# Optimization experiments

Measured on AMD Instinct MI355X. Metric: run time of the kernel, lower is better.

Reference implementation:

```python
import jax, jax.numpy as jnp
import numpy as np

D_MODEL = 128
N_HEADS = 8
D_K = D_MODEL // N_HEADS
N_TGT = 40000
N_SRC = 40000
N_EDGES = 640000


def setup_inputs() -> dict:
    key = jax.random.key(0)
    ks = jax.random.split(key, 12)
    s = 1.0 / np.sqrt(D_MODEL)
    return {
        "X_tgt": jax.random.normal(ks[0], (N_TGT, D_MODEL), jnp.float32),
        "X_src": jax.random.normal(ks[1], (N_SRC, D_MODEL), jnp.float32),
        "inc_tgt": jax.random.randint(ks[2], (N_EDGES,), 0, N_TGT),
        "inc_src": jax.random.randint(ks[3], (N_EDGES,), 0, N_SRC),
        "num_tgt": N_TGT,
        # weights stored (in, out): y = x @ W
        "Wq": jax.random.normal(ks[4], (D_MODEL, D_MODEL), jnp.float32) * s,
        "Wkv": jax.random.normal(ks[5], (D_MODEL, 2 * D_MODEL), jnp.float32) * s,
        "Wbt": jax.random.normal(ks[6], (D_MODEL, N_HEADS), jnp.float32) * s,
        "Wbs": jax.random.normal(ks[7], (D_MODEL, N_HEADS), jnp.float32) * s,
        "Wgt_w": jax.random.normal(ks[8], (D_MODEL, D_MODEL), jnp.float32) * s,
        "Wgt_b": jnp.zeros((D_MODEL,), jnp.float32),
        "Wgs_w": jax.random.normal(ks[9], (D_MODEL, D_MODEL), jnp.float32) * s,
        "Wgs_b": jnp.zeros((D_MODEL,), jnp.float32),
        "Wo": jax.random.normal(ks[10], (D_MODEL, D_MODEL), jnp.float32) * s,
    }


def reference(X_tgt, X_src, inc_tgt, inc_src, num_tgt, Wq, Wkv, Wbt, Wbs,
              Wgt_w, Wgt_b, Wgs_w, Wgs_b, Wo):
    H, dk = N_HEADS, D_K
    scale = 1.0 / np.sqrt(dk)
    n_src = X_src.shape[0]

    Q = (X_tgt @ Wq).reshape(-1, H, dk)                 # [Nt,H,dk]
    kv = (X_src @ Wkv).reshape(n_src, 2, H, dk)
    K, V = kv[:, 0], kv[:, 1]                           # [Ns,H,dk]

    # per-edge attention scores [E,H]
    scores = (jnp.sum(Q[inc_tgt] * K[inc_src], axis=-1) * scale
              + (X_tgt @ Wbt)[inc_tgt]
              + (X_src @ Wbs)[inc_src])

    # segment softmax over edges grouped by target node
    mx = jax.ops.segment_max(scores, inc_tgt, num_segments=num_tgt)  # [Nt,H]
    exp_s = jnp.exp(scores - mx[inc_tgt])
    sm = jax.ops.segment_sum(exp_s, inc_tgt, num_segments=num_tgt)
    attn = exp_s / (sm[inc_tgt] + 1e-12)                # [E,H]

    g_src = jax.nn.sigmoid(X_src @ Wgs_w + Wgs_b).reshape(n_src, H, dk)
    msg = attn[..., None] * (g_src[inc_src] * V[inc_src])          # [E,H,dk]
    out = jax.ops.segment_sum(msg, inc_tgt, num_segments=num_tgt)  # [Nt,H,dk]

    g_tgt = jax.nn.sigmoid(X_tgt @ Wgt_w + Wgt_b).reshape(-1, H, dk)
    return (g_tgt * out).reshape(-1, H * dk) @ Wo
```

## Files before the change

kernel.cpp:

```cpp
#include <hip/hip_runtime.h>
#include <math.h>

#define NTGT 40000
#define NSRC 40000
#define NEDGE 640000
#define LOG2E 1.44269504088896f
#define KGROW 256
#define CAP 64

typedef __attribute__((ext_vector_type(8))) short bfrag;
typedef __attribute__((ext_vector_type(4))) short bhalf4;
typedef __attribute__((ext_vector_type(8))) short bhalf8;
typedef __attribute__((ext_vector_type(4))) float f4acc;

__device__ __forceinline__ ushort f2bf(float f) {
  uint u = __float_as_uint(f);
  u += 0x7fffu + ((u >> 16) & 1u);
  return (ushort)(u >> 16);
}
__device__ __forceinline__ float bflo(uint u) { return __uint_as_float(u << 16); }
__device__ __forceinline__ float bfhi(uint u) { return __uint_as_float(u & 0xffff0000u); }
__device__ __forceinline__ float bf2f(short s) { return __uint_as_float(((uint)(ushort)s) << 16); }
__device__ __forceinline__ float sigmoidf_fast(float x) { return 1.0f / (1.0f + __expf(-x)); }

__global__ __launch_bounds__(256) void k_prep(const float* __restrict__ Wq,
                                              const float* __restrict__ Wkv,
                                              const float* __restrict__ Wgt_w,
                                              const float* __restrict__ Wgs_w,
                                              const float* __restrict__ Wo,
                                              const float* __restrict__ Wbt,
                                              const float* __restrict__ Wbs,
                                              int* __restrict__ cnt,
                                              short* __restrict__ WqT, short* __restrict__ WkT,
                                              short* __restrict__ WvT, short* __restrict__ WgtT,
                                              short* __restrict__ WgsT, short* __restrict__ WoT,
                                              short* __restrict__ WbtT, short* __restrict__ WbsT) {
  const int b = blockIdx.x;
  const int tid = threadIdx.x;
  if (b >= 8) {
    int i = (b - 8) * 256 + tid;
    if (i < NTGT) cnt[i] = 0;
    return;
  }
  if (b >= 6) {
    const float* src = (b == 6) ? Wbt : Wbs;
    short* dst = (b == 6) ? WbtT : WbsT;
    for (int idx = tid; idx < 16 * 128; idx += 256) {
      int n = idx >> 7, k = idx & 127;
      dst[idx] = (n < 8) ? (short)f2bf(src[k * 8 + n]) : (short)0;
    }
    return;
  }
  __shared__ short T[128][136];
  const float* src;
  int ld, off;
  short* dst;
  switch (b) {
    case 0: src = Wq;    ld = 128; off = 0;   dst = WqT;  break;
    case 1: src = Wkv;   ld = 256; off = 0;   dst = WkT;  break;
    case 2: src = Wkv;   ld = 256; off = 128; dst = WvT;  break;
    case 3: src = Wgt_w; ld = 128; off = 0;   dst = WgtT; break;
    case 4: src = Wgs_w; ld = 128; off = 0;   dst = WgsT; break;
    default:src = Wo;    ld = 128; off = 0;   dst = WoT;  break;
  }
  for (int i = tid; i < 128 * 32; i += 256) {
    int k = i >> 5, c4 = (i & 31) * 4;
    float4 v = *reinterpret_cast<const float4*>(src + (size_t)k * ld + off + c4);
    T[c4 + 0][k] = (short)f2bf(v.x);
    T[c4 + 1][k] = (short)f2bf(v.y);
    T[c4 + 2][k] = (short)f2bf(v.z);
    T[c4 + 3][k] = (short)f2bf(v.w);
  }
  __syncthreads();
  for (int u = tid; u < 128 * 16; u += 256) {
    int n = u >> 4, o = (u & 15) * 8;
    *reinterpret_cast<bhalf8*>(dst + (size_t)n * 128 + o) =
        *reinterpret_cast<const bhalf8*>(&T[n][o]);
  }
}

__global__ __launch_bounds__(512) void k_fill(const int* __restrict__ inc_tgt,
                                              const int* __restrict__ inc_src,
                                              int* __restrict__ cnt,
                                              int* __restrict__ elist) {
  int e = blockIdx.x * 512 + threadIdx.x;
  int t = inc_tgt[e];
  int pos = atomicAdd(&cnt[t], 1);
  pos = min(pos, CAP - 1);
  elist[t * CAP + pos] = inc_src[e];
}

#define MFMA16(a, b, c) __builtin_amdgcn_mfma_f32_16x16x32_bf16(a, b, c, 0, 0, 0)

__device__ __forceinline__ void stage_issue(const float* __restrict__ X, size_t row0,
                                            float4 ld[4], int tid) {
#pragma unroll
  for (int it = 0; it < 4; ++it) {
    int i = it * 512 + tid;
    int r = i >> 5, c4 = (i & 31) * 4;
    ld[it] = *reinterpret_cast<const float4*>(X + (row0 + r) * 128 + c4);
  }
}
__device__ __forceinline__ void stage_write(short (*Xs)[136], const float4 ld[4], int tid) {
#pragma unroll
  for (int it = 0; it < 4; ++it) {
    int i = it * 512 + tid;
    int r = i >> 5, c4 = (i & 31) * 4;
    bhalf4 o;
    o[0] = (short)f2bf(ld[it].x); o[1] = (short)f2bf(ld[it].y);
    o[2] = (short)f2bf(ld[it].z); o[3] = (short)f2bf(ld[it].w);
    *reinterpret_cast<bhalf4*>(&Xs[r][c4]) = o;
  }
}

__global__ __launch_bounds__(512) void k_proj(const float* __restrict__ Xt,
                                              const float* __restrict__ Xsrc,
                                              const short* __restrict__ WqT,
                                              const short* __restrict__ WgtT,
                                              const short* __restrict__ WkT,
                                              const short* __restrict__ WvT,
                                              const short* __restrict__ WgsT,
                                              const short* __restrict__ WbtT,
                                              const short* __restrict__ WbsT,
                                              const float* __restrict__ Wgt_b,
                                              const float* __restrict__ Wgs_b,
                                              short* __restrict__ Qb, short* __restrict__ gtb,
                                              float* __restrict__ bt16,
                                              short* __restrict__ KG,
                                              short* __restrict__ bsb) {
  __shared__ short Xs[64][136];
  __shared__ short Stg[64][256];
  const int tid = threadIdx.x;
  const int w = tid >> 6, lane = tid & 63;
  const int nl = lane & 15;
  const int kg = (lane >> 4) * 8;
  const int r4 = (lane >> 4) * 4;
  const int c0 = w * 16;
  const bool is_src = blockIdx.x >= 125;
  const int t0 = (is_src ? blockIdx.x - 125 : blockIdx.x) * 5;
  const float* X = is_src ? Xsrc : Xt;

  if (!is_src) {
    bfrag Bq[4], Bg[4], Bb[4];
#pragma unroll
    for (int ks = 0; ks < 4; ++ks) {
      const size_t wo = (size_t)(c0 + nl) * 128 + ks * 32 + kg;
      Bq[ks] = *reinterpret_cast<const bfrag*>(WqT + wo);
      Bg[ks] = *reinterpret_cast<const bfrag*>(WgtT + wo);
      Bb[ks] = *reinterpret_cast<const bfrag*>(WbtT + (size_t)nl * 128 + ks * 32 + kg);
    }
    const int c = c0 + nl;
    const float gb = Wgt_b[c];
    {
      float4 ld[4];
      stage_issue(X, (size_t)t0 * 64, ld, tid);
      stage_write(Xs, ld, tid);
    }
    __syncthreads();
    for (int ti = 0; ti < 5; ++ti) {
      const size_t row0 = (size_t)(t0 + ti) * 64;
      float4 ld[4];
      if (ti < 4) stage_issue(X, row0 + 64, ld, tid);
      f4acc aQ[4] = {}, aG[4] = {}, aB[4] = {};
#pragma unroll
      for (int ks = 0; ks < 4; ++ks) {
        const int ko = ks * 32 + kg;
        bfrag a0 = *reinterpret_cast<const bfrag*>(&Xs[nl][ko]);
        bfrag a1 = *reinterpret_cast<const bfrag*>(&Xs[16 + nl][ko]);
        bfrag a2 = *reinterpret_cast<const bfrag*>(&Xs[32 + nl][ko]);
        bfrag a3 = *reinterpret_cast<const bfrag*>(&Xs[48 + nl][ko]);
        aQ[0] = MFMA16(a0, Bq[ks], aQ[0]);
        aQ[1] = MFMA16(a1, Bq[ks], aQ[1]);
        aQ[2] = MFMA16(a2, Bq[ks], aQ[2]);
        aQ[3] = MFMA16(a3, Bq[ks], aQ[3]);
        aG[0] = MFMA16(a0, Bg[ks], aG[0]);
        aG[1] = MFMA16(a1, Bg[ks], aG[1]);
        aG[2] = MFMA16(a2, Bg[ks], aG[2]);
        aG[3] = MFMA16(a3, Bg[ks], aG[3]);
        if (w == 0) {
          aB[0] = MFMA16(a0, Bb[ks], aB[0]);
          aB[1] = MFMA16(a1, Bb[ks], aB[1]);
          aB[2] = MFMA16(a2, Bb[ks], aB[2]);
          aB[3] = MFMA16(a3, Bb[ks], aB[3]);
        }
      }
#pragma unroll
      for (int rf = 0; rf < 4; ++rf)
#pragma unroll
        for (int j = 0; j < 4; ++j) {
          int r = rf * 16 + r4 + j;
          Stg[r][c] = (short)f2bf(aQ[rf][j] * (0.25f * LOG2E));
          Stg[r][128 + c] = (short)f2bf(sigmoidf_fast(aG[rf][j] + gb));
        }
      if (w == 0) {
#pragma unroll
        for (int rf = 0; rf < 4; ++rf)
#pragma unroll
          for (int j = 0; j < 4; ++j)
            bt16[(row0 + rf * 16 + r4 + j) * 16 + nl] = aB[rf][j] * LOG2E;
      }
      __syncthreads();
      if (ti < 4) stage_write(Xs, ld, tid);
      for (int u = tid; u < 1024; u += 512) {
        int r = u >> 4, o = (u & 15) * 8;
        *reinterpret_cast<bhalf8*>(Qb + (row0 + r) * 128 + o) =
            *reinterpret_cast<const bhalf8*>(&Stg[r][o]);
        *reinterpret_cast<bhalf8*>(gtb + (row0 + r) * 128 + o) =
            *reinterpret_cast<const bhalf8*>(&Stg[r][128 + o]);
      }
      __syncthreads();
    }
  } else {
    bfrag Bk[4], Bv[4], Bg[4], Bb[4];
#pragma unroll
    for (int ks = 0; ks < 4; ++ks) {
      const size_t wo = (size_t)(c0 + nl) * 128 + ks * 32 + kg;
      Bk[ks] = *reinterpret_cast<const bfrag*>(WkT + wo);
      Bv[ks] = *reinterpret_cast<const bfrag*>(WvT + wo);
      Bg[ks] = *reinterpret_cast<const bfrag*>(WgsT + wo);
      Bb[ks] = *reinterpret_cast<const bfrag*>(WbsT + (size_t)nl * 128 + ks * 32 + kg);
    }
    const int c = c0 + nl;
    const int slot = (c >> 1) * 4 + (c & 1);
    const float gb = Wgs_b[c];
    {
      float4 ld[4];
      stage_issue(X, (size_t)t0 * 64, ld, tid);
      stage_write(Xs, ld, tid);
    }
    __syncthreads();
    for (int ti = 0; ti < 5; ++ti) {
      const size_t row0 = (size_t)(t0 + ti) * 64;
      float4 ld[4];
      if (ti < 4) stage_issue(X, row0 + 64, ld, tid);
      f4acc aK[4] = {}, aV[4] = {}, aG[4] = {}, aB[4] = {};
#pragma unroll
      for (int ks = 0; ks < 4; ++ks) {
        const int ko = ks * 32 + kg;
        bfrag a0 = *reinterpret_cast<const bfrag*>(&Xs[nl][ko]);
        bfrag a1 = *reinterpret_cast<const bfrag*>(&Xs[16 + nl][ko]);
        bfrag a2 = *reinterpret_cast<const bfrag*>(&Xs[32 + nl][ko]);
        bfrag a3 = *reinterpret_cast<const bfrag*>(&Xs[48 + nl][ko]);
        aK[0] = MFMA16(a0, Bk[ks], aK[0]);
        aK[1] = MFMA16(a1, Bk[ks], aK[1]);
        aK[2] = MFMA16(a2, Bk[ks], aK[2]);
        aK[3] = MFMA16(a3, Bk[ks], aK[3]);
        aV[0] = MFMA16(a0, Bv[ks], aV[0]);
        aV[1] = MFMA16(a1, Bv[ks], aV[1]);
        aV[2] = MFMA16(a2, Bv[ks], aV[2]);
        aV[3] = MFMA16(a3, Bv[ks], aV[3]);
        aG[0] = MFMA16(a0, Bg[ks], aG[0]);
        aG[1] = MFMA16(a1, Bg[ks], aG[1]);
        aG[2] = MFMA16(a2, Bg[ks], aG[2]);
        aG[3] = MFMA16(a3, Bg[ks], aG[3]);
        if (w == 0) {
          aB[0] = MFMA16(a0, Bb[ks], aB[0]);
          aB[1] = MFMA16(a1, Bb[ks], aB[1]);
          aB[2] = MFMA16(a2, Bb[ks], aB[2]);
          aB[3] = MFMA16(a3, Bb[ks], aB[3]);
        }
      }
#pragma unroll
      for (int rf = 0; rf < 4; ++rf)
#pragma unroll
        for (int j = 0; j < 4; ++j) {
          int r = rf * 16 + r4 + j;
          float g = sigmoidf_fast(aG[rf][j] + gb);
          Stg[r][slot] = (short)f2bf(aK[rf][j]);
          Stg[r][slot + 2] = (short)f2bf(g * aV[rf][j]);
        }
      if (w == 0 && nl < 8) {
#pragma unroll
        for (int rf = 0; rf < 4; ++rf)
#pragma unroll
          for (int j = 0; j < 4; ++j)
            bsb[(row0 + rf * 16 + r4 + j) * 8 + nl] = (short)f2bf(aB[rf][j] * LOG2E);
      }
      __syncthreads();
      if (ti < 4) stage_write(Xs, ld, tid);
      for (int u = tid; u < 2048; u += 512) {
        int r = u >> 5, o = (u & 31) * 8;
        *reinterpret_cast<bhalf8*>(KG + (row0 + r) * KGROW + o) =
            *reinterpret_cast<const bhalf8*>(&Stg[r][o]);
      }
      __syncthreads();
    }
  }
}

__global__ __launch_bounds__(256) void k_attn(const uint2* __restrict__ Qp2,
                                              const uint4* __restrict__ KGp4,
                                              const float* __restrict__ bt16,
                                              const short* __restrict__ bsb,
                                              const uint2* __restrict__ gtp2,
                                              const int* __restrict__ cnt,
                                              const int* __restrict__ elist,
                                              uint2* __restrict__ tmpp2) {
  const int wave = threadIdx.x >> 6;
  const int lane = threadIdx.x & 63;
  const int t = blockIdx.x * 4 + wave;
  const int p = lane & 31;
  const int h = p >> 2;
  const int hi = lane >> 5;

  uint2 qv = Qp2[(size_t)t * 32 + p];
  float q0 = bflo(qv.x), q1 = bfhi(qv.x), q2 = bflo(qv.y), q3 = bfhi(qv.y);
  const float bt2 = bt16[(size_t)t * 16 + h];
  const int deg = cnt[t];
  const int ebase = t * CAP;

  float ssum = 0.f, a0 = 0.f, a1 = 0.f, a2 = 0.f, a3 = 0.f;
  int i = 0;
  for (; i + 8 <= deg; i += 8) {
    int sv[4];
    uint4 kv[4];
    float bv[4], dd[4];
#pragma unroll
    for (int u = 0; u < 4; ++u) sv[u] = elist[ebase + i + 2 * u + hi];
#pragma unroll
    for (int u = 0; u < 4; ++u) {
      kv[u] = KGp4[(size_t)sv[u] * 32 + p];
      bv[u] = bf2f(bsb[(size_t)sv[u] * 8 + h]);
    }
#pragma unroll
    for (int u = 0; u < 4; ++u)
      dd[u] = q0 * bflo(kv[u].x) + q1 * bfhi(kv[u].x) + q2 * bflo(kv[u].z) + q3 * bfhi(kv[u].z);
#pragma unroll
    for (int u = 0; u < 4; ++u) dd[u] += __shfl_xor(dd[u], 1);
#pragma unroll
    for (int u = 0; u < 4; ++u) dd[u] += __shfl_xor(dd[u], 2);
#pragma unroll
    for (int u = 0; u < 4; ++u) {
      float e = __builtin_amdgcn_exp2f(dd[u] + bt2 + bv[u]);
      ssum += e;
      a0 = fmaf(e, bflo(kv[u].y), a0);
      a1 = fmaf(e, bfhi(kv[u].y), a1);
      a2 = fmaf(e, bflo(kv[u].w), a2);
      a3 = fmaf(e, bfhi(kv[u].w), a3);
    }
  }
  for (; i < deg; i += 2) {
    int idx = i + hi;
    float pen = 0.f;
    if (idx >= deg) { idx = deg - 1; pen = -1e30f; }
    int s = elist[ebase + idx];
    uint4 kv = KGp4[(size_t)s * 32 + p];
    float bsv = bf2f(bsb[(size_t)s * 8 + h]);
    float d = q0 * bflo(kv.x) + q1 * bfhi(kv.x) + q2 * bflo(kv.z) + q3 * bfhi(kv.z);
    d += __shfl_xor(d, 1);
    d += __shfl_xor(d, 2);
    float e = __builtin_amdgcn_exp2f(d + bt2 + bsv + pen);
    ssum += e;
    a0 = fmaf(e, bflo(kv.y), a0);
    a1 = fmaf(e, bfhi(kv.y), a1);
    a2 = fmaf(e, bflo(kv.w), a2);
    a3 = fmaf(e, bfhi(kv.w), a3);
  }
  ssum += __shfl_xor(ssum, 32);
  a0 += __shfl_xor(a0, 32);
  a1 += __shfl_xor(a1, 32);
  a2 += __shfl_xor(a2, 32);
  a3 += __shfl_xor(a3, 32);
  if (lane < 32) {
    float inv = 1.f / (ssum + 1e-12f);
    uint2 g2 = gtp2[(size_t)t * 32 + p];
    float o0 = bflo(g2.x) * a0 * inv;
    float o1 = bfhi(g2.x) * a1 * inv;
    float o2 = bflo(g2.y) * a2 * inv;
    float o3 = bfhi(g2.y) * a3 * inv;
    uint2 pk;
    pk.x = ((uint)f2bf(o0)) | (((uint)f2bf(o1)) << 16);
    pk.y = ((uint)f2bf(o2)) | (((uint)f2bf(o3)) << 16);
    tmpp2[(size_t)t * 32 + p] = pk;
  }
}

__device__ __forceinline__ void stage_rows_bf16(const short* __restrict__ X, size_t row0,
                                                short (*Xs)[136], int tid) {
  for (int i = tid; i < 64 * 32; i += 256) {
    int r = i >> 5, c4 = (i & 31) * 4;
    *reinterpret_cast<bhalf4*>(&Xs[r][c4]) =
        *reinterpret_cast<const bhalf4*>(X + (row0 + r) * 128 + c4);
  }
}

__device__ __forceinline__ void mfma_pass(const short (*Xs)[136], int wave, int lane,
                                          const short* __restrict__ WT, f4acc acc[8]) {
  const int rl = wave * 16 + (lane & 15);
  const int kg = (lane >> 4) * 8;
  const int nl = lane & 15;
#pragma unroll
  for (int ks = 0; ks < 4; ++ks) {
    bfrag a = *reinterpret_cast<const bfrag*>(&Xs[rl][ks * 32 + kg]);
#pragma unroll
    for (int nf = 0; nf < 8; ++nf) {
      bfrag b = *reinterpret_cast<const bfrag*>(WT + (size_t)(nf * 16 + nl) * 128 + ks * 32 + kg);
      acc[nf] = MFMA16(a, b, acc[nf]);
    }
  }
}

__global__ __launch_bounds__(256) void k_out(const short* __restrict__ tmpb,
                                             const short* __restrict__ WoT,
                                             float* __restrict__ out) {
  __shared__ short Xs[64][136];
  const int tid = threadIdx.x;
  const size_t row0 = (size_t)blockIdx.x * 64;
  stage_rows_bf16(tmpb, row0, Xs, tid);
  __syncthreads();
  const int wave = tid >> 6, lane = tid & 63;
  const int rbase = (int)row0 + wave * 16 + ((lane >> 4) << 2);
  const int cl = lane & 15;
  f4acc acc[8] = {};
  mfma_pass(Xs, wave, lane, WoT, acc);
#pragma unroll
  for (int nf = 0; nf < 8; ++nf)
#pragma unroll
    for (int j = 0; j < 4; ++j)
      out[(size_t)(rbase + j) * 128 + nf * 16 + cl] = acc[nf][j];
}

extern "C" void kernel_launch(void* const* d_in, const int* in_sizes, int n_in,
                              void* d_out, int out_size, void* d_ws, size_t ws_size,
                              hipStream_t stream) {
  const float* X_tgt = (const float*)d_in[0];
  const float* X_src = (const float*)d_in[1];
  const int* inc_tgt = (const int*)d_in[2];
  const int* inc_src = (const int*)d_in[3];
  const float* Wq    = (const float*)d_in[5];
  const float* Wkv   = (const float*)d_in[6];
  const float* Wbt   = (const float*)d_in[7];
  const float* Wbs   = (const float*)d_in[8];
  const float* Wgt_w = (const float*)d_in[9];
  const float* Wgt_b = (const float*)d_in[10];
  const float* Wgs_w = (const float*)d_in[11];
  const float* Wgs_b = (const float*)d_in[12];
  const float* Wo    = (const float*)d_in[13];
  float* out = (float*)d_out;

  char* ws = (char*)d_ws;
  short* Qb   = (short*)ws; ws += (size_t)NTGT * 128 * 2;
  short* KG   = (short*)ws; ws += (size_t)NSRC * KGROW * 2;
  short* gtb  = (short*)ws; ws += (size_t)NTGT * 128 * 2;
  short* tmpb = (short*)ws; ws += (size_t)NTGT * 128 * 2;
  float* bt16 = (float*)ws; ws += (size_t)NTGT * 16 * 4;
  short* bsb  = (short*)ws; ws += (size_t)NSRC * 8 * 2;
  int* cnt   = (int*)ws; ws += (size_t)NTGT * 4;
  int* elist = (int*)ws; ws += (size_t)NTGT * CAP * 4;
  short* WqT  = (short*)ws; ws += 128 * 128 * 2;
  short* WkT  = (short*)ws; ws += 128 * 128 * 2;
  short* WvT  = (short*)ws; ws += 128 * 128 * 2;
  short* WgtT = (short*)ws; ws += 128 * 128 * 2;
  short* WgsT = (short*)ws; ws += 128 * 128 * 2;
  short* WoT  = (short*)ws; ws += 128 * 128 * 2;
  short* WbtT = (short*)ws; ws += 16 * 128 * 2;
  short* WbsT = (short*)ws; ws += 16 * 128 * 2;

  k_prep<<<165, 256, 0, stream>>>(Wq, Wkv, Wgt_w, Wgs_w, Wo, Wbt, Wbs, cnt,
                                  WqT, WkT, WvT, WgtT, WgsT, WoT, WbtT, WbsT);
  k_fill<<<NEDGE / 512, 512, 0, stream>>>(inc_tgt, inc_src, cnt, elist);
  k_proj<<<250, 512, 0, stream>>>(X_tgt, X_src, WqT, WgtT, WkT, WvT, WgsT,
                                  WbtT, WbsT, Wgt_b, Wgs_b,
                                  Qb, gtb, bt16, KG, bsb);
  k_attn<<<NTGT / 4, 256, 0, stream>>>((const uint2*)Qb, (const uint4*)KG, bt16, bsb,
                                       (const uint2*)gtb, cnt, elist, (uint2*)tmpb);
  k_out<<<NTGT / 64, 256, 0, stream>>>(tmpb, WoT, out);
}
```

Measured before the change: 146.9 us.

## Fuse edge bucketing into projection kernel and pad counters to avoid contention

Removes the separate k_fill launch and appends 1250 extra blocks to k_proj that do the atomic edge bucketing. These blocks can run alongside the projection GEMM blocks, and one kernel launch is saved. Per-target counters are padded to a 64-byte stride so atomics on neighbouring targets no longer share cache lines. The cost is a 16x larger counter array that k_prep must zero with many more blocks, and the degree read in k_attn is now clamped to CAP.

```diff
diff --git a/kernel.cpp b/kernel.cpp
--- a/kernel.cpp
+++ b/kernel.cpp
@@ -30,7 +30,7 @@
                                               const float* __restrict__ Wo,
                                               const float* __restrict__ Wbt,
                                               const float* __restrict__ Wbs,
-                                              int* __restrict__ cnt,
+                                              int* __restrict__ cntp,
                                               short* __restrict__ WqT, short* __restrict__ WkT,
                                               short* __restrict__ WvT, short* __restrict__ WgtT,
                                               short* __restrict__ WgsT, short* __restrict__ WoT,
@@ -38,8 +38,9 @@
   const int b = blockIdx.x;
   const int tid = threadIdx.x;
   if (b >= 8) {
-    int i = (b - 8) * 256 + tid;
-    if (i < NTGT) cnt[i] = 0;
+    int i = (b - 8) * 1024 + tid * 4;
+    int4 z = {0, 0, 0, 0};
+    *reinterpret_cast<int4*>(cntp + i) = z;
     return;
   }
   if (b >= 6) {
@@ -79,17 +80,6 @@
   }
 }
 
-__global__ __launch_bounds__(512) void k_fill(const int* __restrict__ inc_tgt,
-                                              const int* __restrict__ inc_src,
-                                              int* __restrict__ cnt,
-                                              int* __restrict__ elist) {
-  int e = blockIdx.x * 512 + threadIdx.x;
-  int t = inc_tgt[e];
-  int pos = atomicAdd(&cnt[t], 1);
-  pos = min(pos, CAP - 1);
-  elist[t * CAP + pos] = inc_src[e];
-}
-
 #define MFMA16(a, b, c) __builtin_amdgcn_mfma_f32_16x16x32_bf16(a, b, c, 0, 0, 0)
 
 __device__ __forceinline__ void stage_issue(const float* __restrict__ X, size_t row0,
@@ -124,13 +114,25 @@
                                               const short* __restrict__ WbsT,
                                               const float* __restrict__ Wgt_b,
                                               const float* __restrict__ Wgs_b,
+                                              const int* __restrict__ inc_tgt,
+                                              const int* __restrict__ inc_src,
+                                              int* __restrict__ cntp,
+                                              int* __restrict__ elist,
                                               short* __restrict__ Qb, short* __restrict__ gtb,
                                               float* __restrict__ bt16,
                                               short* __restrict__ KG,
                                               short* __restrict__ bsb) {
+  const int tid = threadIdx.x;
+  if (blockIdx.x >= 250) {
+    int e = (blockIdx.x - 250) * 512 + tid;
+    int t = inc_tgt[e];
+    int pos = atomicAdd(&cntp[t << 4], 1);
+    pos = min(pos, CAP - 1);
+    elist[t * CAP + pos] = inc_src[e];
+    return;
+  }
   __shared__ short Xs[64][136];
   __shared__ short Stg[64][256];
-  const int tid = threadIdx.x;
   const int w = tid >> 6, lane = tid & 63;
   const int nl = lane & 15;
   const int kg = (lane >> 4) * 8;
@@ -293,7 +295,7 @@
                                               const float* __restrict__ bt16,
                                               const short* __restrict__ bsb,
                                               const uint2* __restrict__ gtp2,
-                                              const int* __restrict__ cnt,
+                                              const int* __restrict__ cntp,
                                               const int* __restrict__ elist,
                                               uint2* __restrict__ tmpp2) {
   const int wave = threadIdx.x >> 6;
@@ -306,7 +308,7 @@
   uint2 qv = Qp2[(size_t)t * 32 + p];
   float q0 = bflo(qv.x), q1 = bfhi(qv.x), q2 = bflo(qv.y), q3 = bfhi(qv.y);
   const float bt2 = bt16[(size_t)t * 16 + h];
-  const int deg = cnt[t];
+  const int deg = min(cntp[t << 4], CAP);
   const int ebase = t * CAP;
 
   float ssum = 0.f, a0 = 0.f, a1 = 0.f, a2 = 0.f, a3 = 0.f;
@@ -445,7 +447,7 @@
   short* tmpb = (short*)ws; ws += (size_t)NTGT * 128 * 2;
   float* bt16 = (float*)ws; ws += (size_t)NTGT * 16 * 4;
   short* bsb  = (short*)ws; ws += (size_t)NSRC * 8 * 2;
-  int* cnt   = (int*)ws; ws += (size_t)NTGT * 4;
+  int* cntp  = (int*)ws; ws += (size_t)NTGT * 16 * 4;
   int* elist = (int*)ws; ws += (size_t)NTGT * CAP * 4;
   short* WqT  = (short*)ws; ws += 128 * 128 * 2;
   short* WkT  = (short*)ws; ws += 128 * 128 * 2;
@@ -456,13 +458,13 @@
   short* WbtT = (short*)ws; ws += 16 * 128 * 2;
   short* WbsT = (short*)ws; ws += 16 * 128 * 2;
 
-  k_prep<<<165, 256, 0, stream>>>(Wq, Wkv, Wgt_w, Wgs_w, Wo, Wbt, Wbs, cnt,
+  k_prep<<<633, 256, 0, stream>>>(Wq, Wkv, Wgt_w, Wgs_w, Wo, Wbt, Wbs, cntp,
                                   WqT, WkT, WvT, WgtT, WgsT, WoT, WbtT, WbsT);
-  k_fill<<<NEDGE / 512, 512, 0, stream>>>(inc_tgt, inc_src, cnt, elist);
-  k_proj<<<250, 512, 0, stream>>>(X_tgt, X_src, WqT, WgtT, WkT, WvT, WgsT,
-                                  WbtT, WbsT, Wgt_b, Wgs_b,
-                                  Qb, gtb, bt16, KG, bsb);
+  k_proj<<<1500, 512, 0, stream>>>(X_tgt, X_src, WqT, WgtT, WkT, WvT, WgsT,
+                                   WbtT, WbsT, Wgt_b, Wgs_b,
+                                   inc_tgt, inc_src, cntp, elist,
+                                   Qb, gtb, bt16, KG, bsb);
   k_attn<<<NTGT / 4, 256, 0, stream>>>((const uint2*)Qb, (const uint4*)KG, bt16, bsb,
-                                       (const uint2*)gtb, cnt, elist, (uint2*)tmpb);
+                                       (const uint2*)gtb, cntp, elist, (uint2*)tmpb);
   k_out<<<NTGT / 64, 256, 0, stream>>>(tmpb, WoT, out);
 }
```

After: 147.6 us. About the same (+0.4%).
